# Optimization experiments

Measured on AMD Instinct MI355X. Metric: run time of the kernel, lower is better.

The kernel has to match this reference:

```python
import jax, jax.numpy as jnp
import numpy as np

D_MODEL = 128
N_HEADS = 8
D_K = D_MODEL // N_HEADS
N_NODES = 50000
N_EDGES = 800000


def setup_inputs() -> dict:
    key = jax.random.key(0)
    ks = jax.random.split(key, 8)
    X = jax.random.normal(ks[0], (N_NODES, D_MODEL), dtype=jnp.float32)
    nbr_src = jax.random.randint(ks[1], (N_EDGES,), 0, N_NODES, dtype=jnp.int32)
    nbr_dst = jax.random.randint(ks[2], (N_EDGES,), 0, N_NODES, dtype=jnp.int32)
    s = 1.0 / np.sqrt(D_MODEL)
    W_qkv = jax.random.normal(ks[3], (3 * D_MODEL, D_MODEL), dtype=jnp.float32) * s
    w_bias = jax.random.normal(ks[4], (N_HEADS, D_MODEL), dtype=jnp.float32) * s
    W_gate = jax.random.normal(ks[5], (D_MODEL, D_MODEL), dtype=jnp.float32) * s
    b_gate = jax.random.normal(ks[6], (D_MODEL,), dtype=jnp.float32) * s
    W_o = jax.random.normal(ks[7], (D_MODEL, D_MODEL), dtype=jnp.float32) * s
    return {"X": X, "W_qkv": W_qkv, "w_bias": w_bias, "W_gate": W_gate,
            "b_gate": b_gate, "W_o": W_o, "nbr_src": nbr_src,
            "nbr_dst": nbr_dst, "num_cells": N_NODES}


def segment_softmax(scores, seg, num_segments):
    # scores: [E, H], seg: [E] -> softmax over edges sharing the same seg id
    mx = jax.ops.segment_max(scores, seg, num_segments=num_segments)  # [N, H]
    mx = jnp.where(jnp.isfinite(mx), mx, -1e9)
    exp_s = jnp.exp(scores - mx[seg])
    sm = jax.ops.segment_sum(exp_s, seg, num_segments=num_segments)  # [N, H]
    return exp_s / (sm[seg] + 1e-12)


def reference(X, W_qkv, w_bias, W_gate, b_gate, W_o, nbr_src, nbr_dst, num_cells):
    H, dk = N_HEADS, D_K
    scale = 1.0 / np.sqrt(dk)
    qkv = (X @ W_qkv.T).reshape(-1, 3, H, dk)      # [N, 3, H, dk]
    Q, K, V = qkv[:, 0], qkv[:, 1], qkv[:, 2]
    gate = jax.nn.sigmoid(X @ W_gate.T + b_gate).reshape(-1, H, dk)
    bias = X @ w_bias.T                             # [N, H]
    scores = jnp.einsum('ehd,ehd->eh', Q[nbr_src], K[nbr_dst]) * scale + bias[nbr_src]
    attn = segment_softmax(scores, nbr_src, num_cells)          # [E, H]
    out = jax.ops.segment_sum(attn[:, :, None] * V[nbr_dst], nbr_src,
                              num_segments=num_cells)           # [N, H, dk]
    return (gate * out).reshape(-1, D_MODEL) @ W_o.T
```

## Files before the change

kernel.cpp:

```cpp
#include <hip/hip_runtime.h>
#include <hip/hip_fp16.h>

#define DM 128
#define NHEADS 8
#define MAXDEG 64
#define SROW 136

typedef _Float16 half8 __attribute__((ext_vector_type(8)));
typedef _Float16 half2v __attribute__((ext_vector_type(2)));
typedef float floatx4 __attribute__((ext_vector_type(4)));

union H8 { half8 v; half2v h2[4]; };

__global__ __launch_bounds__(256) void proj_csr(
    const float* __restrict__ X, const float* __restrict__ Wqkv,
    const float* __restrict__ Wgate, const float* __restrict__ wbias,
    const float* __restrict__ b_gate,
    const int* __restrict__ nsrc, const int* __restrict__ ndst,
    int* __restrict__ cnt, int* __restrict__ csr_dst,
    _Float16* __restrict__ Q, _Float16* __restrict__ KV,
    _Float16* __restrict__ gate, float* __restrict__ bias,
    int M, int E, int P) {
  __shared__ _Float16 As[128 * SROW];
  __shared__ _Float16 Bs[64 * SROW];
  int tid = threadIdx.x;
  int bid = blockIdx.x;

  if (bid >= P) {
    int ebase = (bid - P) * 8192;
    for (int g = 0; g < 4; g++) {
      int s[8], d[8];
#pragma unroll
      for (int j = 0; j < 8; j++) {
        int e = ebase + (g * 8 + j) * 256 + tid;
        s[j] = (e < E) ? nsrc[e] : -1;
        d[j] = (e < E) ? ndst[e] : 0;
      }
#pragma unroll
      for (int j = 0; j < 8; j++) {
        if (s[j] >= 0) {
          int p = atomicAdd(&cnt[s[j]], 1);
          if (p < MAXDEG) csr_dst[(size_t)s[j] * MAXDEG + p] = d[j];
        }
      }
    }
    return;
  }

  int m0 = bid * 128;

#pragma unroll
  for (int i = 0; i < 4; i++) {
    int u = tid + i * 256;
    int r = u >> 3;
    int cc = (u & 7) * 16;
    int gr = m0 + r;
    float4 f0, f1, f2, f3;
    if (gr < M) {
      const float4* src = (const float4*)(X + (size_t)gr * 128 + cc);
      f0 = src[0]; f1 = src[1]; f2 = src[2]; f3 = src[3];
    } else {
      f0 = f1 = f2 = f3 = make_float4(0.f, 0.f, 0.f, 0.f);
    }
    half8 h0 = {(_Float16)f0.x, (_Float16)f0.y, (_Float16)f0.z, (_Float16)f0.w,
                (_Float16)f1.x, (_Float16)f1.y, (_Float16)f1.z, (_Float16)f1.w};
    half8 h1 = {(_Float16)f2.x, (_Float16)f2.y, (_Float16)f2.z, (_Float16)f2.w,
                (_Float16)f3.x, (_Float16)f3.y, (_Float16)f3.z, (_Float16)f3.w};
    *(half8*)(As + r * SROW + cc) = h0;
    *(half8*)(As + r * SROW + cc + 8) = h1;
  }

  int wid = tid >> 6, lane = tid & 63;
  int quad = lane >> 4, l16 = lane & 15;
  int mw = wid * 32;

  for (int c = 0; c < 9; c++) {
    __syncthreads();
#pragma unroll
    for (int i = 0; i < 4; i++) {
      int u = tid + i * 256;
      int r = u >> 4;
      int cc = (u & 15) * 8;
      int grow = c * 64 + r;
      const float* src = nullptr;
      if (grow < 384)      src = Wqkv + (size_t)grow * 128 + cc;
      else if (grow < 512) src = Wgate + (size_t)(grow - 384) * 128 + cc;
      else if (grow < 520) src = wbias + (size_t)(grow - 512) * 128 + cc;
      half8 h = {};
      if (src) {
        float4 f0 = ((const float4*)src)[0];
        float4 f1 = ((const float4*)src)[1];
        h = half8{(_Float16)f0.x, (_Float16)f0.y, (_Float16)f0.z, (_Float16)f0.w,
                  (_Float16)f1.x, (_Float16)f1.y, (_Float16)f1.z, (_Float16)f1.w};
      }
      *(half8*)(Bs + r * SROW + cc) = h;
    }
    __syncthreads();

    floatx4 acc[2][4] = {};
#pragma unroll
    for (int kc = 0; kc < 4; kc++) {
      int ko = kc * 32 + quad * 8;
      half8 a0 = *(const half8*)(As + (mw + l16) * SROW + ko);
      half8 a1 = *(const half8*)(As + (mw + 16 + l16) * SROW + ko);
      half8 b[4];
#pragma unroll
      for (int ni = 0; ni < 4; ni++)
        b[ni] = *(const half8*)(Bs + (ni * 16 + l16) * SROW + ko);
#pragma unroll
      for (int ni = 0; ni < 4; ni++) {
        acc[0][ni] = __builtin_amdgcn_mfma_f32_16x16x32_f16(a0, b[ni], acc[0][ni], 0, 0, 0);
        acc[1][ni] = __builtin_amdgcn_mfma_f32_16x16x32_f16(a1, b[ni], acc[1][ni], 0, 0, 0);
      }
    }

    if (c == 8) {
      if (l16 < 8) {
#pragma unroll
        for (int mi = 0; mi < 2; mi++)
#pragma unroll
          for (int r = 0; r < 4; r++) {
            int row = m0 + mw + mi * 16 + quad * 4 + r;
            if (row < M) bias[(size_t)row * 8 + l16] = acc[mi][0][r];
          }
      }
    } else {
      int reg = c >> 1;
#pragma unroll
      for (int mi = 0; mi < 2; mi++) {
#pragma unroll
        for (int ni = 0; ni < 4; ni++) {
          int colL = (c & 1) * 64 + ni * 16 + l16;
#pragma unroll
          for (int r = 0; r < 4; r++) {
            int row = m0 + mw + mi * 16 + quad * 4 + r;
            if (row >= M) continue;
            float v = acc[mi][ni][r];
            if (reg == 0)      Q[(size_t)row * 128 + colL] = (_Float16)v;
            else if (reg == 1) KV[(size_t)row * 256 + colL] = (_Float16)v;
            else if (reg == 2) KV[(size_t)row * 256 + 128 + colL] = (_Float16)v;
            else gate[(size_t)row * 128 + colL] =
                   (_Float16)(1.0f / (1.0f + __expf(-(v + b_gate[colL]))));
          }
        }
      }
    }
  }
}

__global__ __launch_bounds__(256) void final_gemm_mfma(
    const _Float16* __restrict__ A, const float* __restrict__ Wo,
    float* __restrict__ C, int M) {
  __shared__ _Float16 As[128 * SROW];
  __shared__ _Float16 Bs[64 * SROW];
  int tid = threadIdx.x;
  int m0 = blockIdx.x * 128, n0 = blockIdx.y * 64;
#pragma unroll
  for (int i = 0; i < 8; i++) {
    int u = tid + i * 256;
    int r = u >> 4;
    int cc = (u & 15) * 8;
    int gr = m0 + r;
    int4 val = make_int4(0, 0, 0, 0);
    if (gr < M) val = *(const int4*)(A + (size_t)gr * 128 + cc);
    *(int4*)(As + r * SROW + cc) = val;
  }
#pragma unroll
  for (int i = 0; i < 4; i++) {
    int u = tid + i * 256;
    int r = u >> 4;
    int cc = (u & 15) * 8;
    const float* src = Wo + (size_t)(n0 + r) * 128 + cc;
    float4 f0 = ((const float4*)src)[0];
    float4 f1 = ((const float4*)src)[1];
    half8 h = {(_Float16)f0.x, (_Float16)f0.y, (_Float16)f0.z, (_Float16)f0.w,
               (_Float16)f1.x, (_Float16)f1.y, (_Float16)f1.z, (_Float16)f1.w};
    *(half8*)(Bs + r * SROW + cc) = h;
  }
  __syncthreads();

  int wid = tid >> 6, lane = tid & 63;
  int quad = lane >> 4, l16 = lane & 15;
  int mw = (wid >> 1) * 64;
  int nw = (wid & 1) * 32;

  floatx4 acc[4][2] = {};
#pragma unroll
  for (int kc = 0; kc < 4; kc++) {
    int ko = kc * 32 + quad * 8;
    half8 a[4], b[2];
#pragma unroll
    for (int mi = 0; mi < 4; mi++)
      a[mi] = *(const half8*)(As + (mw + mi * 16 + l16) * SROW + ko);
#pragma unroll
    for (int ni = 0; ni < 2; ni++)
      b[ni] = *(const half8*)(Bs + (nw + ni * 16 + l16) * SROW + ko);
#pragma unroll
    for (int mi = 0; mi < 4; mi++)
#pragma unroll
      for (int ni = 0; ni < 2; ni++)
        acc[mi][ni] = __builtin_amdgcn_mfma_f32_16x16x32_f16(a[mi], b[ni], acc[mi][ni], 0, 0, 0);
  }
#pragma unroll
  for (int mi = 0; mi < 4; mi++) {
#pragma unroll
    for (int ni = 0; ni < 2; ni++) {
      int col = n0 + nw + ni * 16 + l16;
#pragma unroll
      for (int r = 0; r < 4; r++) {
        int row = m0 + mw + mi * 16 + quad * 4 + r;
        if (row >= M) continue;
        C[(size_t)row * 128 + col] = acc[mi][ni][r];
      }
    }
  }
}

__global__ __launch_bounds__(256) void attn_fused(
    const int* __restrict__ cnt, const int* __restrict__ csr_dst,
    const _Float16* __restrict__ Q, const _Float16* __restrict__ KV,
    const float* __restrict__ bias, const _Float16* __restrict__ gate,
    _Float16* __restrict__ gated, int N) {
  int wave = threadIdx.x >> 6, lane = threadIdx.x & 63;
  int n = blockIdx.x * 4 + wave;
  if (n >= N) return;
  int deg = cnt[n];
  if (deg > MAXDEG) deg = MAXDEG;
  int qtr = lane >> 4, l16 = lane & 15;
  int ch0 = l16 * 8;

  int dstv = csr_dst[(size_t)n * MAXDEG + lane];

  H8 qu; qu.v = *(const half8*)(Q + (size_t)n * DM + ch0);
  float bias_h = bias[(size_t)n * NHEADS + (l16 >> 1)];

  float acc[8] = {};
  float den = 0.f;
  int iters = (deg + 3) >> 2;

  H8 k0, v0, k1, v1;
  k0.v = half8{}; v0.v = half8{}; k1.v = half8{}; v1.v = half8{};
  bool b0 = false, b1 = false;
  if (0 < iters) {
    int e = qtr;
    b0 = e < deg;
    int d = __shfl(dstv, e);
    d = b0 ? d : 0;
    const _Float16* kvp = KV + (size_t)d * 256 + ch0;
    k0.v = *(const half8*)kvp;
    v0.v = *(const half8*)(kvp + 128);
  }
  if (1 < iters) {
    int e = 4 + qtr;
    b1 = e < deg;
    int d = __shfl(dstv, e);
    d = b1 ? d : 0;
    const _Float16* kvp = KV + (size_t)d * 256 + ch0;
    k1.v = *(const half8*)kvp;
    v1.v = *(const half8*)(kvp + 128);
  }

  for (int it = 0; it < iters; it++) {
    H8 k2, v2;
    k2.v = half8{}; v2.v = half8{};
    bool b2 = false;
    if (it + 2 < iters) {
      int e = (it + 2) * 4 + qtr;
      b2 = e < deg;
      int d = __shfl(dstv, e);
      d = b2 ? d : 0;
      const _Float16* kvp = KV + (size_t)d * 256 + ch0;
      k2.v = *(const half8*)kvp;
      v2.v = *(const half8*)(kvp + 128);
    }
    float p = 0.f;
#pragma unroll
    for (int j = 0; j < 4; j++)
      p = __builtin_amdgcn_fdot2(qu.h2[j], k0.h2[j], p, false);
    p += __shfl_xor(p, 1);
    float w = __expf(p * 0.25f + bias_h);
    if (!b0) w = 0.f;
    den += w;
#pragma unroll
    for (int j = 0; j < 8; j++) acc[j] = fmaf(w, (float)v0.v[j], acc[j]);
    k0 = k1; v0 = v1; b0 = b1;
    k1 = k2; v1 = v2; b1 = b2;
  }
#pragma unroll
  for (int j = 0; j < 8; j++) acc[j] += __shfl_xor(acc[j], 16);
#pragma unroll
  for (int j = 0; j < 8; j++) acc[j] += __shfl_xor(acc[j], 32);
  den += __shfl_xor(den, 16);
  den += __shfl_xor(den, 32);

  if (qtr == 0) {
    float inv = 1.0f / (den + 1e-12f);
    half8 gv = *(const half8*)(gate + (size_t)n * DM + ch0);
    half8 o;
#pragma unroll
    for (int j = 0; j < 8; j++) o[j] = (_Float16)(acc[j] * inv * (float)gv[j]);
    *(half8*)(gated + (size_t)n * DM + ch0) = o;
  }
}

extern "C" void kernel_launch(void* const* d_in, const int* in_sizes, int n_in,
                              void* d_out, int out_size, void* d_ws, size_t ws_size,
                              hipStream_t stream) {
  const float* X     = (const float*)d_in[0];
  const float* Wqkv  = (const float*)d_in[1];
  const float* wbias = (const float*)d_in[2];
  const float* Wgate = (const float*)d_in[3];
  const float* bgate = (const float*)d_in[4];
  const float* Wo    = (const float*)d_in[5];
  const int*   nsrc  = (const int*)d_in[6];
  const int*   ndst  = (const int*)d_in[7];
  int N = in_sizes[0] / 128;
  int E = in_sizes[6];
  float* out = (float*)d_out;

  char* p = (char*)d_ws;
  _Float16* Q16     = (_Float16*)p; p += (size_t)N * 128 * sizeof(_Float16);
  _Float16* KV16    = (_Float16*)p; p += (size_t)N * 256 * sizeof(_Float16);
  _Float16* gate16  = (_Float16*)p; p += (size_t)N * 128 * sizeof(_Float16);
  _Float16* gated16 = (_Float16*)p; p += (size_t)N * 128 * sizeof(_Float16);
  float* bias       = (float*)p;    p += (size_t)N * 8 * sizeof(float);
  int* cnt          = (int*)p;      p += (size_t)N * sizeof(int);
  int* csr_dst      = (int*)p;      p += (size_t)N * MAXDEG * sizeof(int);

  hipMemsetAsync(cnt, 0, (size_t)N * sizeof(int), stream);

  int P = (N + 127) / 128;
  int C = (E + 8191) / 8192;
  proj_csr<<<P + C, 256, 0, stream>>>(X, Wqkv, Wgate, wbias, bgate, nsrc, ndst,
                                      cnt, csr_dst, Q16, KV16, gate16, bias, N, E, P);

  attn_fused<<<(N + 3) / 4, 256, 0, stream>>>(cnt, csr_dst, Q16, KV16, bias,
                                              gate16, gated16, N);

  dim3 fg((N + 127) / 128, 2);
  final_gemm_mfma<<<fg, 256, 0, stream>>>(gated16, Wo, out, N);
}
```

Before: 217.4 us.

## Fuse attention aggregation with output projection and regrid CSR build

Merges the attention kernel and the final W_o GEMM into one kernel. Each 1024-thread block handles 16 nodes, writes the gated outputs to shared memory and multiplies them by W_o with MFMA, so the gated fp16 intermediate never goes through global memory and one launch is removed. Each lane now covers a full 16-channel head, which drops the per-head shuffle, and 8 edges are processed per iteration. The CSR build now uses one edge per thread across many more blocks. The cost is that every block converts and stages all of W_o (about 35KB of LDS), and half the waves sit idle during the GEMM phase.

After: 240.9 us. 10.8% more time.

```diff
diff --git a/kernel.cpp b/kernel.cpp
--- a/kernel.cpp
+++ b/kernel.cpp
@@ -10,7 +10,7 @@
 typedef _Float16 half2v __attribute__((ext_vector_type(2)));
 typedef float floatx4 __attribute__((ext_vector_type(4)));
 
-union H8 { half8 v; half2v h2[4]; };
+union H16 { half8 v8[2]; half2v h2[8]; _Float16 h[16]; };
 
 __global__ __launch_bounds__(256) void proj_csr(
     const float* __restrict__ X, const float* __restrict__ Wqkv,
@@ -27,22 +27,12 @@
   int bid = blockIdx.x;
 
   if (bid >= P) {
-    int ebase = (bid - P) * 8192;
-    for (int g = 0; g < 4; g++) {
-      int s[8], d[8];
-#pragma unroll
-      for (int j = 0; j < 8; j++) {
-        int e = ebase + (g * 8 + j) * 256 + tid;
-        s[j] = (e < E) ? nsrc[e] : -1;
-        d[j] = (e < E) ? ndst[e] : 0;
-      }
-#pragma unroll
-      for (int j = 0; j < 8; j++) {
-        if (s[j] >= 0) {
-          int p = atomicAdd(&cnt[s[j]], 1);
-          if (p < MAXDEG) csr_dst[(size_t)s[j] * MAXDEG + p] = d[j];
-        }
-      }
+    int e = (bid - P) * 256 + tid;
+    if (e < E) {
+      int s = nsrc[e];
+      int d = ndst[e];
+      int p = atomicAdd(&cnt[s], 1);
+      if (p < MAXDEG) csr_dst[(size_t)s * MAXDEG + p] = d;
     }
     return;
   }
@@ -148,158 +138,139 @@
   }
 }
 
-__global__ __launch_bounds__(256) void final_gemm_mfma(
-    const _Float16* __restrict__ A, const float* __restrict__ Wo,
-    float* __restrict__ C, int M) {
-  __shared__ _Float16 As[128 * SROW];
-  __shared__ _Float16 Bs[64 * SROW];
-  int tid = threadIdx.x;
-  int m0 = blockIdx.x * 128, n0 = blockIdx.y * 64;
-#pragma unroll
-  for (int i = 0; i < 8; i++) {
-    int u = tid + i * 256;
-    int r = u >> 4;
-    int cc = (u & 15) * 8;
-    int gr = m0 + r;
-    int4 val = make_int4(0, 0, 0, 0);
-    if (gr < M) val = *(const int4*)(A + (size_t)gr * 128 + cc);
-    *(int4*)(As + r * SROW + cc) = val;
-  }
-#pragma unroll
-  for (int i = 0; i < 4; i++) {
-    int u = tid + i * 256;
-    int r = u >> 4;
-    int cc = (u & 15) * 8;
-    const float* src = Wo + (size_t)(n0 + r) * 128 + cc;
-    float4 f0 = ((const float4*)src)[0];
-    float4 f1 = ((const float4*)src)[1];
-    half8 h = {(_Float16)f0.x, (_Float16)f0.y, (_Float16)f0.z, (_Float16)f0.w,
-               (_Float16)f1.x, (_Float16)f1.y, (_Float16)f1.z, (_Float16)f1.w};
-    *(half8*)(Bs + r * SROW + cc) = h;
-  }
-  __syncthreads();
-
-  int wid = tid >> 6, lane = tid & 63;
-  int quad = lane >> 4, l16 = lane & 15;
-  int mw = (wid >> 1) * 64;
-  int nw = (wid & 1) * 32;
-
-  floatx4 acc[4][2] = {};
-#pragma unroll
-  for (int kc = 0; kc < 4; kc++) {
-    int ko = kc * 32 + quad * 8;
-    half8 a[4], b[2];
-#pragma unroll
-    for (int mi = 0; mi < 4; mi++)
-      a[mi] = *(const half8*)(As + (mw + mi * 16 + l16) * SROW + ko);
-#pragma unroll
-    for (int ni = 0; ni < 2; ni++)
-      b[ni] = *(const half8*)(Bs + (nw + ni * 16 + l16) * SROW + ko);
-#pragma unroll
-    for (int mi = 0; mi < 4; mi++)
-#pragma unroll
-      for (int ni = 0; ni < 2; ni++)
-        acc[mi][ni] = __builtin_amdgcn_mfma_f32_16x16x32_f16(a[mi], b[ni], acc[mi][ni], 0, 0, 0);
-  }
-#pragma unroll
-  for (int mi = 0; mi < 4; mi++) {
-#pragma unroll
-    for (int ni = 0; ni < 2; ni++) {
-      int col = n0 + nw + ni * 16 + l16;
-#pragma unroll
-      for (int r = 0; r < 4; r++) {
-        int row = m0 + mw + mi * 16 + quad * 4 + r;
-        if (row >= M) continue;
-        C[(size_t)row * 128 + col] = acc[mi][ni][r];
-      }
-    }
-  }
-}
-
-__global__ __launch_bounds__(256) void attn_fused(
+__global__ __launch_bounds__(1024) void attn_out(
     const int* __restrict__ cnt, const int* __restrict__ csr_dst,
     const _Float16* __restrict__ Q, const _Float16* __restrict__ KV,
     const float* __restrict__ bias, const _Float16* __restrict__ gate,
-    _Float16* __restrict__ gated, int N) {
-  int wave = threadIdx.x >> 6, lane = threadIdx.x & 63;
-  int n = blockIdx.x * 4 + wave;
-  if (n >= N) return;
-  int deg = cnt[n];
+    const float* __restrict__ Wo, float* __restrict__ out, int N) {
+  __shared__ _Float16 Ws[128 * SROW];
+  __shared__ _Float16 Gs[16 * SROW];
+  int tid = threadIdx.x;
+
+#pragma unroll
+  for (int i = 0; i < 2; i++) {
+    int u = tid + i * 1024;
+    int r = u >> 4;
+    int cc = (u & 15) * 8;
+    const float4* s = (const float4*)(Wo + (size_t)r * 128 + cc);
+    float4 f0 = s[0], f1 = s[1];
+    half8 h = {(_Float16)f0.x, (_Float16)f0.y, (_Float16)f0.z, (_Float16)f0.w,
+               (_Float16)f1.x, (_Float16)f1.y, (_Float16)f1.z, (_Float16)f1.w};
+    *(half8*)(Ws + r * SROW + cc) = h;
+  }
+
+  int wid = tid >> 6, lane = tid & 63;
+  int n0 = blockIdx.x * 16;
+  int n = n0 + wid;
+  bool active = n < N;
+  int n_eff = active ? n : 0;
+  int g = lane >> 3, h = lane & 7;
+  int ch0 = h * 16;
+
+  int deg = active ? cnt[n_eff] : 0;
   if (deg > MAXDEG) deg = MAXDEG;
-  int qtr = lane >> 4, l16 = lane & 15;
-  int ch0 = l16 * 8;
-
-  int dstv = csr_dst[(size_t)n * MAXDEG + lane];
-
-  H8 qu; qu.v = *(const half8*)(Q + (size_t)n * DM + ch0);
-  float bias_h = bias[(size_t)n * NHEADS + (l16 >> 1)];
-
-  float acc[8] = {};
+  int dstv = csr_dst[(size_t)n_eff * MAXDEG + lane];
+
+  H16 qu;
+  qu.v8[0] = *(const half8*)(Q + (size_t)n_eff * DM + ch0);
+  qu.v8[1] = *(const half8*)(Q + (size_t)n_eff * DM + ch0 + 8);
+  float bias_h = bias[(size_t)n_eff * NHEADS + h];
+
+  float acc[16] = {};
   float den = 0.f;
-  int iters = (deg + 3) >> 2;
-
-  H8 k0, v0, k1, v1;
-  k0.v = half8{}; v0.v = half8{}; k1.v = half8{}; v1.v = half8{};
+  int iters = (deg + 7) >> 3;
+
+  H16 k0, v0, k1, v1;
+  k0.v8[0] = half8{}; k0.v8[1] = half8{};
+  v0.v8[0] = half8{}; v0.v8[1] = half8{};
+  k1 = k0; v1 = v0;
   bool b0 = false, b1 = false;
   if (0 < iters) {
-    int e = qtr;
+    int e = g;
     b0 = e < deg;
     int d = __shfl(dstv, e);
     d = b0 ? d : 0;
     const _Float16* kvp = KV + (size_t)d * 256 + ch0;
-    k0.v = *(const half8*)kvp;
-    v0.v = *(const half8*)(kvp + 128);
+    k0.v8[0] = *(const half8*)kvp;       k0.v8[1] = *(const half8*)(kvp + 8);
+    v0.v8[0] = *(const half8*)(kvp + 128); v0.v8[1] = *(const half8*)(kvp + 136);
   }
   if (1 < iters) {
-    int e = 4 + qtr;
+    int e = 8 + g;
     b1 = e < deg;
     int d = __shfl(dstv, e);
     d = b1 ? d : 0;
     const _Float16* kvp = KV + (size_t)d * 256 + ch0;
-    k1.v = *(const half8*)kvp;
-    v1.v = *(const half8*)(kvp + 128);
+    k1.v8[0] = *(const half8*)kvp;       k1.v8[1] = *(const half8*)(kvp + 8);
+    v1.v8[0] = *(const half8*)(kvp + 128); v1.v8[1] = *(const half8*)(kvp + 136);
   }
 
   for (int it = 0; it < iters; it++) {
-    H8 k2, v2;
-    k2.v = half8{}; v2.v = half8{};
+    H16 k2, v2;
+    k2.v8[0] = half8{}; k2.v8[1] = half8{};
+    v2.v8[0] = half8{}; v2.v8[1] = half8{};
     bool b2 = false;
     if (it + 2 < iters) {
-      int e = (it + 2) * 4 + qtr;
+      int e = (it + 2) * 8 + g;
       b2 = e < deg;
       int d = __shfl(dstv, e);
       d = b2 ? d : 0;
       const _Float16* kvp = KV + (size_t)d * 256 + ch0;
-      k2.v = *(const half8*)kvp;
-      v2.v = *(const half8*)(kvp + 128);
+      k2.v8[0] = *(const half8*)kvp;       k2.v8[1] = *(const half8*)(kvp + 8);
+      v2.v8[0] = *(const half8*)(kvp + 128); v2.v8[1] = *(const half8*)(kvp + 136);
     }
     float p = 0.f;
 #pragma unroll
-    for (int j = 0; j < 4; j++)
+    for (int j = 0; j < 8; j++)
       p = __builtin_amdgcn_fdot2(qu.h2[j], k0.h2[j], p, false);
-    p += __shfl_xor(p, 1);
     float w = __expf(p * 0.25f + bias_h);
     if (!b0) w = 0.f;
     den += w;
 #pragma unroll
-    for (int j = 0; j < 8; j++) acc[j] = fmaf(w, (float)v0.v[j], acc[j]);
+    for (int j = 0; j < 16; j++) acc[j] = fmaf(w, (float)v0.h[j], acc[j]);
     k0 = k1; v0 = v1; b0 = b1;
     k1 = k2; v1 = v2; b1 = b2;
   }
 #pragma unroll
-  for (int j = 0; j < 8; j++) acc[j] += __shfl_xor(acc[j], 16);
-#pragma unroll
-  for (int j = 0; j < 8; j++) acc[j] += __shfl_xor(acc[j], 32);
+  for (int j = 0; j < 16; j++) {
+    acc[j] += __shfl_xor(acc[j], 8);
+    acc[j] += __shfl_xor(acc[j], 16);
+    acc[j] += __shfl_xor(acc[j], 32);
+  }
+  den += __shfl_xor(den, 8);
   den += __shfl_xor(den, 16);
   den += __shfl_xor(den, 32);
 
-  if (qtr == 0) {
+  if (g == 0) {
     float inv = 1.0f / (den + 1e-12f);
-    half8 gv = *(const half8*)(gate + (size_t)n * DM + ch0);
-    half8 o;
-#pragma unroll
-    for (int j = 0; j < 8; j++) o[j] = (_Float16)(acc[j] * inv * (float)gv[j]);
-    *(half8*)(gated + (size_t)n * DM + ch0) = o;
+    H16 gv;
+    gv.v8[0] = *(const half8*)(gate + (size_t)n_eff * DM + ch0);
+    gv.v8[1] = *(const half8*)(gate + (size_t)n_eff * DM + ch0 + 8);
+    H16 o;
+#pragma unroll
+    for (int j = 0; j < 16; j++)
+      o.h[j] = active ? (_Float16)(acc[j] * inv * (float)gv.h[j]) : (_Float16)0.f;
+    *(half8*)(Gs + wid * SROW + ch0) = o.v8[0];
+    *(half8*)(Gs + wid * SROW + ch0 + 8) = o.v8[1];
+  }
+
+  __syncthreads();
+
+  if (wid < 8) {
+    int quad = lane >> 4, l16 = lane & 15;
+    floatx4 oc = {};
+#pragma unroll
+    for (int kc = 0; kc < 4; kc++) {
+      int ko = kc * 32 + quad * 8;
+      half8 a = *(const half8*)(Gs + l16 * SROW + ko);
+      half8 b = *(const half8*)(Ws + (wid * 16 + l16) * SROW + ko);
+      oc = __builtin_amdgcn_mfma_f32_16x16x32_f16(a, b, oc, 0, 0, 0);
+    }
+    int col = wid * 16 + l16;
+#pragma unroll
+    for (int r = 0; r < 4; r++) {
+      int row = n0 + quad * 4 + r;
+      if (row < N) out[(size_t)row * 128 + col] = oc[r];
+    }
   }
 }
 
@@ -322,7 +293,6 @@
   _Float16* Q16     = (_Float16*)p; p += (size_t)N * 128 * sizeof(_Float16);
   _Float16* KV16    = (_Float16*)p; p += (size_t)N * 256 * sizeof(_Float16);
   _Float16* gate16  = (_Float16*)p; p += (size_t)N * 128 * sizeof(_Float16);
-  _Float16* gated16 = (_Float16*)p; p += (size_t)N * 128 * sizeof(_Float16);
   float* bias       = (float*)p;    p += (size_t)N * 8 * sizeof(float);
   int* cnt          = (int*)p;      p += (size_t)N * sizeof(int);
   int* csr_dst      = (int*)p;      p += (size_t)N * MAXDEG * sizeof(int);
@@ -330,13 +300,10 @@
   hipMemsetAsync(cnt, 0, (size_t)N * sizeof(int), stream);
 
   int P = (N + 127) / 128;
-  int C = (E + 8191) / 8192;
+  int C = (E + 255) / 256;
   proj_csr<<<P + C, 256, 0, stream>>>(X, Wqkv, Wgate, wbias, bgate, nsrc, ndst,
                                       cnt, csr_dst, Q16, KV16, gate16, bias, N, E, P);
 
-  attn_fused<<<(N + 3) / 4, 256, 0, stream>>>(cnt, csr_dst, Q16, KV16, bias,
-                                              gate16, gated16, N);
-
-  dim3 fg((N + 127) / 128, 2);
-  final_gemm_mfma<<<fg, 256, 0, stream>>>(gated16, Wo, out, N);
+  attn_out<<<(N + 15) / 16, 1024, 0, stream>>>(cnt, csr_dst, Q16, KV16, bias,
+                                               gate16, Wo, out, N);
 }
```

## Fuse output projection into attention kernel and pre-convert Wo to fp16

Applied to the files above, without the earlier changes.

Removes the separate final GEMM kernel. Each attention block now writes its 4 gated node rows into shared memory and multiplies them by an fp16 copy of W_o using MFMA, writing fp32 output directly. This drops the global write and re-read of the gated intermediate and one kernel launch. The W_o fp16 conversion is done by a few extra blocks in the projection kernel. The cost is that each block reloads a 32KB W_o slice from cache, uses only 4 of 16 MFMA rows, and adds a block-wide sync.

New measurement: 243.3 us. +11.9%, slower.

```diff
diff --git a/kernel.cpp b/kernel.cpp
--- a/kernel.cpp
+++ b/kernel.cpp
@@ -5,26 +5,40 @@
 #define NHEADS 8
 #define MAXDEG 64
 #define SROW 136
+#define WCONV_BLOCKS 8
 
 typedef _Float16 half8 __attribute__((ext_vector_type(8)));
 typedef _Float16 half2v __attribute__((ext_vector_type(2)));
 typedef float floatx4 __attribute__((ext_vector_type(4)));
 
-union H8 { half8 v; half2v h2[4]; };
+union H8 { half8 v; half2v h2[4]; _Float16 h[8]; };
+
+__device__ inline half8 cvt8(const float4 f0, const float4 f1) {
+  return half8{(_Float16)f0.x, (_Float16)f0.y, (_Float16)f0.z, (_Float16)f0.w,
+               (_Float16)f1.x, (_Float16)f1.y, (_Float16)f1.z, (_Float16)f1.w};
+}
 
 __global__ __launch_bounds__(256) void proj_csr(
     const float* __restrict__ X, const float* __restrict__ Wqkv,
     const float* __restrict__ Wgate, const float* __restrict__ wbias,
-    const float* __restrict__ b_gate,
+    const float* __restrict__ b_gate, const float* __restrict__ Wo,
     const int* __restrict__ nsrc, const int* __restrict__ ndst,
     int* __restrict__ cnt, int* __restrict__ csr_dst,
     _Float16* __restrict__ Q, _Float16* __restrict__ KV,
     _Float16* __restrict__ gate, float* __restrict__ bias,
-    int M, int E, int P) {
+    _Float16* __restrict__ Wo16,
+    int M, int E, int P, int C) {
   __shared__ _Float16 As[128 * SROW];
   __shared__ _Float16 Bs[64 * SROW];
   int tid = threadIdx.x;
   int bid = blockIdx.x;
+
+  if (bid >= P + C) {
+    int u = (bid - P - C) * 2048 + tid * 8;
+    const float4* s = (const float4*)(Wo + u);
+    *(half8*)(Wo16 + u) = cvt8(s[0], s[1]);
+    return;
+  }
 
   if (bid >= P) {
     int ebase = (bid - P) * 8192;
@@ -62,12 +76,8 @@
     } else {
       f0 = f1 = f2 = f3 = make_float4(0.f, 0.f, 0.f, 0.f);
     }
-    half8 h0 = {(_Float16)f0.x, (_Float16)f0.y, (_Float16)f0.z, (_Float16)f0.w,
-                (_Float16)f1.x, (_Float16)f1.y, (_Float16)f1.z, (_Float16)f1.w};
-    half8 h1 = {(_Float16)f2.x, (_Float16)f2.y, (_Float16)f2.z, (_Float16)f2.w,
-                (_Float16)f3.x, (_Float16)f3.y, (_Float16)f3.z, (_Float16)f3.w};
-    *(half8*)(As + r * SROW + cc) = h0;
-    *(half8*)(As + r * SROW + cc + 8) = h1;
+    *(half8*)(As + r * SROW + cc) = cvt8(f0, f1);
+    *(half8*)(As + r * SROW + cc + 8) = cvt8(f2, f3);
   }
 
   int wid = tid >> 6, lane = tid & 63;
@@ -87,12 +97,7 @@
       else if (grow < 512) src = Wgate + (size_t)(grow - 384) * 128 + cc;
       else if (grow < 520) src = wbias + (size_t)(grow - 512) * 128 + cc;
       half8 h = {};
-      if (src) {
-        float4 f0 = ((const float4*)src)[0];
-        float4 f1 = ((const float4*)src)[1];
-        h = half8{(_Float16)f0.x, (_Float16)f0.y, (_Float16)f0.z, (_Float16)f0.w,
-                  (_Float16)f1.x, (_Float16)f1.y, (_Float16)f1.z, (_Float16)f1.w};
-      }
+      if (src) h = cvt8(((const float4*)src)[0], ((const float4*)src)[1]);
       *(half8*)(Bs + r * SROW + cc) = h;
     }
     __syncthreads();
@@ -148,91 +153,27 @@
   }
 }
 
-__global__ __launch_bounds__(256) void final_gemm_mfma(
-    const _Float16* __restrict__ A, const float* __restrict__ Wo,
-    float* __restrict__ C, int M) {
-  __shared__ _Float16 As[128 * SROW];
-  __shared__ _Float16 Bs[64 * SROW];
-  int tid = threadIdx.x;
-  int m0 = blockIdx.x * 128, n0 = blockIdx.y * 64;
-#pragma unroll
-  for (int i = 0; i < 8; i++) {
-    int u = tid + i * 256;
-    int r = u >> 4;
-    int cc = (u & 15) * 8;
-    int gr = m0 + r;
-    int4 val = make_int4(0, 0, 0, 0);
-    if (gr < M) val = *(const int4*)(A + (size_t)gr * 128 + cc);
-    *(int4*)(As + r * SROW + cc) = val;
-  }
-#pragma unroll
-  for (int i = 0; i < 4; i++) {
-    int u = tid + i * 256;
-    int r = u >> 4;
-    int cc = (u & 15) * 8;
-    const float* src = Wo + (size_t)(n0 + r) * 128 + cc;
-    float4 f0 = ((const float4*)src)[0];
-    float4 f1 = ((const float4*)src)[1];
-    half8 h = {(_Float16)f0.x, (_Float16)f0.y, (_Float16)f0.z, (_Float16)f0.w,
-               (_Float16)f1.x, (_Float16)f1.y, (_Float16)f1.z, (_Float16)f1.w};
-    *(half8*)(Bs + r * SROW + cc) = h;
-  }
-  __syncthreads();
-
-  int wid = tid >> 6, lane = tid & 63;
-  int quad = lane >> 4, l16 = lane & 15;
-  int mw = (wid >> 1) * 64;
-  int nw = (wid & 1) * 32;
-
-  floatx4 acc[4][2] = {};
-#pragma unroll
-  for (int kc = 0; kc < 4; kc++) {
-    int ko = kc * 32 + quad * 8;
-    half8 a[4], b[2];
-#pragma unroll
-    for (int mi = 0; mi < 4; mi++)
-      a[mi] = *(const half8*)(As + (mw + mi * 16 + l16) * SROW + ko);
-#pragma unroll
-    for (int ni = 0; ni < 2; ni++)
-      b[ni] = *(const half8*)(Bs + (nw + ni * 16 + l16) * SROW + ko);
-#pragma unroll
-    for (int mi = 0; mi < 4; mi++)
-#pragma unroll
-      for (int ni = 0; ni < 2; ni++)
-        acc[mi][ni] = __builtin_amdgcn_mfma_f32_16x16x32_f16(a[mi], b[ni], acc[mi][ni], 0, 0, 0);
-  }
-#pragma unroll
-  for (int mi = 0; mi < 4; mi++) {
-#pragma unroll
-    for (int ni = 0; ni < 2; ni++) {
-      int col = n0 + nw + ni * 16 + l16;
-#pragma unroll
-      for (int r = 0; r < 4; r++) {
-        int row = m0 + mw + mi * 16 + quad * 4 + r;
-        if (row >= M) continue;
-        C[(size_t)row * 128 + col] = acc[mi][ni][r];
-      }
-    }
-  }
-}
-
-__global__ __launch_bounds__(256) void attn_fused(
+__global__ __launch_bounds__(256) void attn_out(
     const int* __restrict__ cnt, const int* __restrict__ csr_dst,
     const _Float16* __restrict__ Q, const _Float16* __restrict__ KV,
     const float* __restrict__ bias, const _Float16* __restrict__ gate,
-    _Float16* __restrict__ gated, int N) {
+    const _Float16* __restrict__ Wo16, float* __restrict__ out, int N) {
+  __shared__ _Float16 Gs[16 * SROW];
   int wave = threadIdx.x >> 6, lane = threadIdx.x & 63;
-  int n = blockIdx.x * 4 + wave;
-  if (n >= N) return;
-  int deg = cnt[n];
-  if (deg > MAXDEG) deg = MAXDEG;
+  int n0 = blockIdx.x * 4;
+  int n = n0 + wave;
+  bool active = n < N;
+  int n_eff = active ? n : 0;
   int qtr = lane >> 4, l16 = lane & 15;
   int ch0 = l16 * 8;
 
-  int dstv = csr_dst[(size_t)n * MAXDEG + lane];
-
-  H8 qu; qu.v = *(const half8*)(Q + (size_t)n * DM + ch0);
-  float bias_h = bias[(size_t)n * NHEADS + (l16 >> 1)];
+  int deg = active ? cnt[n_eff] : 0;
+  if (deg > MAXDEG) deg = MAXDEG;
+
+  int dstv = csr_dst[(size_t)n_eff * MAXDEG + lane];
+
+  H8 qu; qu.v = *(const half8*)(Q + (size_t)n_eff * DM + ch0);
+  float bias_h = bias[(size_t)n_eff * NHEADS + (l16 >> 1)];
 
   float acc[8] = {};
   float den = 0.f;
@@ -261,8 +202,7 @@
   }
 
   for (int it = 0; it < iters; it++) {
-    H8 k2, v2;
-    k2.v = half8{}; v2.v = half8{};
+    H8 k2, v2; k2.v = half8{}; v2.v = half8{};
     bool b2 = false;
     if (it + 2 < iters) {
       int e = (it + 2) * 4 + qtr;
@@ -282,24 +222,50 @@
     if (!b0) w = 0.f;
     den += w;
 #pragma unroll
-    for (int j = 0; j < 8; j++) acc[j] = fmaf(w, (float)v0.v[j], acc[j]);
+    for (int j = 0; j < 8; j++) acc[j] = fmaf(w, (float)v0.h[j], acc[j]);
     k0 = k1; v0 = v1; b0 = b1;
     k1 = k2; v1 = v2; b1 = b2;
   }
 #pragma unroll
-  for (int j = 0; j < 8; j++) acc[j] += __shfl_xor(acc[j], 16);
-#pragma unroll
-  for (int j = 0; j < 8; j++) acc[j] += __shfl_xor(acc[j], 32);
+  for (int j = 0; j < 8; j++) {
+    acc[j] += __shfl_xor(acc[j], 16);
+    acc[j] += __shfl_xor(acc[j], 32);
+  }
   den += __shfl_xor(den, 16);
   den += __shfl_xor(den, 32);
 
   if (qtr == 0) {
     float inv = 1.0f / (den + 1e-12f);
-    half8 gv = *(const half8*)(gate + (size_t)n * DM + ch0);
+    H8 gv; gv.v = *(const half8*)(gate + (size_t)n_eff * DM + ch0);
     half8 o;
 #pragma unroll
-    for (int j = 0; j < 8; j++) o[j] = (_Float16)(acc[j] * inv * (float)gv[j]);
-    *(half8*)(gated + (size_t)n * DM + ch0) = o;
+    for (int j = 0; j < 8; j++) o[j] = (_Float16)(acc[j] * inv * (float)gv.h[j]);
+    *(half8*)(Gs + wave * SROW + ch0) = o;
+  }
+
+  __syncthreads();
+
+  floatx4 oc[2] = {};
+#pragma unroll
+  for (int kc = 0; kc < 4; kc++) {
+    int ko = kc * 32 + qtr * 8;
+    half8 a = *(const half8*)(Gs + l16 * SROW + ko);
+#pragma unroll
+    for (int ni = 0; ni < 2; ni++) {
+      half8 b = *(const half8*)(Wo16 + (size_t)(wave * 32 + ni * 16 + l16) * 128 + ko);
+      oc[ni] = __builtin_amdgcn_mfma_f32_16x16x32_f16(a, b, oc[ni], 0, 0, 0);
+    }
+  }
+  if (qtr == 0) {
+#pragma unroll
+    for (int ni = 0; ni < 2; ni++) {
+      int col = wave * 32 + ni * 16 + l16;
+#pragma unroll
+      for (int r = 0; r < 4; r++) {
+        int row = n0 + r;
+        if (row < N) out[(size_t)row * 128 + col] = oc[ni][r];
+      }
+    }
   }
 }
 
@@ -322,8 +288,8 @@
   _Float16* Q16     = (_Float16*)p; p += (size_t)N * 128 * sizeof(_Float16);
   _Float16* KV16    = (_Float16*)p; p += (size_t)N * 256 * sizeof(_Float16);
   _Float16* gate16  = (_Float16*)p; p += (size_t)N * 128 * sizeof(_Float16);
-  _Float16* gated16 = (_Float16*)p; p += (size_t)N * 128 * sizeof(_Float16);
   float* bias       = (float*)p;    p += (size_t)N * 8 * sizeof(float);
+  _Float16* Wo16    = (_Float16*)p; p += (size_t)128 * 128 * sizeof(_Float16);
   int* cnt          = (int*)p;      p += (size_t)N * sizeof(int);
   int* csr_dst      = (int*)p;      p += (size_t)N * MAXDEG * sizeof(int);
 
@@ -331,12 +297,10 @@
 
   int P = (N + 127) / 128;
   int C = (E + 8191) / 8192;
-  proj_csr<<<P + C, 256, 0, stream>>>(X, Wqkv, Wgate, wbias, bgate, nsrc, ndst,
-                                      cnt, csr_dst, Q16, KV16, gate16, bias, N, E, P);
-
-  attn_fused<<<(N + 3) / 4, 256, 0, stream>>>(cnt, csr_dst, Q16, KV16, bias,
-                                              gate16, gated16, N);
-
-  dim3 fg((N + 127) / 128, 2);
-  final_gemm_mfma<<<fg, 256, 0, stream>>>(gated16, Wo, out, N);
+  proj_csr<<<P + C + WCONV_BLOCKS, 256, 0, stream>>>(
+      X, Wqkv, Wgate, wbias, bgate, Wo, nsrc, ndst,
+      cnt, csr_dst, Q16, KV16, gate16, bias, Wo16, N, E, P, C);
+
+  attn_out<<<(N + 3) / 4, 256, 0, stream>>>(cnt, csr_dst, Q16, KV16, bias,
+                                            gate16, Wo16, out, N);
 }
```
